# Kernel tuning notes

Hardware: AMD Instinct MI355X
Metric: run time of the kernel (lower is better)

Reference implementation:

```python
import jax, jax.numpy as jnp
import numpy as np


def setup_inputs() -> dict:
    key = jax.random.key(0)
    k1, k2, k3, k4 = jax.random.split(key, 4)
    N, E, F_IN, H, C = 100000, 1600000, 128, 64, 64
    x = jax.random.normal(k1, (N, F_IN), dtype=jnp.float32)
    edge_index = jax.random.randint(k2, (2, E), 0, N, dtype=jnp.int64)
    W1 = jax.random.normal(k3, (F_IN, H), dtype=jnp.float32) / np.sqrt(F_IN)
    b1 = jnp.zeros((H,), dtype=jnp.float32)
    W2 = jax.random.normal(k4, (H, C), dtype=jnp.float32) / np.sqrt(H)
    b2 = jnp.zeros((C,), dtype=jnp.float32)
    return {"x": x, "edge_index": edge_index, "W1": W1, "b1": b1, "W2": W2, "b2": b2}


def reference(x, edge_index, W1, b1, W2, b2):
    N = x.shape[0]
    # add self-loops (PyG GCNConv default)
    loop = jnp.arange(N, dtype=edge_index.dtype)
    src = jnp.concatenate([edge_index[0], loop])
    dst = jnp.concatenate([edge_index[1], loop])
    # symmetric normalization: deg^{-1/2}[src] * deg^{-1/2}[dst], deg over dst
    deg = jax.ops.segment_sum(jnp.ones_like(dst, dtype=x.dtype), dst, num_segments=N)
    dis = jnp.where(deg > 0, jax.lax.rsqrt(deg), 0.0)
    norm = dis[src] * dis[dst]  # [E+N]

    def gcn_conv(h, W, b):
        h = h @ W                                   # [N, out]
        msg = h[src] * norm[:, None]                # [E+N, out] gather
        agg = jax.ops.segment_sum(msg, dst, num_segments=N)  # scatter-add
        return agg + b

    h = jax.nn.relu(gcn_conv(x, W1, b1))
    # dropout inactive in eval mode
    out = gcn_conv(h, W2, b2)
    return jax.nn.log_softmax(out, axis=1)
```

## Files before the change

### kernel.cpp

```cpp
#include <hip/hip_runtime.h>
#include <cstdint>
#include <cstddef>

#define PASSA_EDGES 2048

typedef __attribute__((ext_vector_type(8))) short bf16x8;
typedef __attribute__((ext_vector_type(4))) float f32x4;


__device__ __forceinline__ unsigned short f2bf(float f) {
    unsigned int u = __float_as_uint(f);
    u += 0x7FFFu + ((u >> 16) & 1u);
    return (unsigned short)(u >> 16);
}
__device__ __forceinline__ float bf2f(unsigned short h) {
    return __uint_as_float((unsigned int)h << 16);
}

__device__ __forceinline__ void bf8_fma(uint4 u, float w, float* acc) {
    acc[0] += __uint_as_float(u.x << 16) * w;
    acc[1] += __uint_as_float(u.x & 0xFFFF0000u) * w;
    acc[2] += __uint_as_float(u.y << 16) * w;
    acc[3] += __uint_as_float(u.y & 0xFFFF0000u) * w;
    acc[4] += __uint_as_float(u.z << 16) * w;
    acc[5] += __uint_as_float(u.z & 0xFFFF0000u) * w;
    acc[6] += __uint_as_float(u.w << 16) * w;
    acc[7] += __uint_as_float(u.w & 0xFFFF0000u) * w;
}
__device__ __forceinline__ void bf8_unpack(uint4 u, float* v) {
    v[0] = __uint_as_float(u.x << 16);
    v[1] = __uint_as_float(u.x & 0xFFFF0000u);
    v[2] = __uint_as_float(u.y << 16);
    v[3] = __uint_as_float(u.y & 0xFFFF0000u);
    v[4] = __uint_as_float(u.z << 16);
    v[5] = __uint_as_float(u.z & 0xFFFF0000u);
    v[6] = __uint_as_float(u.w << 16);
    v[7] = __uint_as_float(u.w & 0xFFFF0000u);
}


__global__ void bcur_init(int* __restrict__ bcur, int NBUCK, int CAP) {
    int b = threadIdx.x;
    if (b < NBUCK) bcur[b] = b * CAP;
}


__global__ __launch_bounds__(256) void passA(const int* __restrict__ src,
                                             const int* __restrict__ dst,
                                             int* __restrict__ bcur,
                                             int2* __restrict__ bbuf, int E,
                                             int CAP, int shift) {
    __shared__ int cnt[256], cur[256];
    const int t  = threadIdx.x;
    const int e0 = blockIdx.x * PASSA_EDGES;
    const int n  = min(PASSA_EDGES, E - e0);

    cnt[t] = 0;
    __syncthreads();
    for (int i = t; i < n; i += 256) atomicAdd(&cnt[dst[e0 + i] >> shift], 1);
    __syncthreads();

    const int c = cnt[t];
    cur[t] = (c > 0) ? atomicAdd(&bcur[t], c) : 0;
    __syncthreads();

    for (int i = t; i < n; i += 256) {
        const int d = dst[e0 + i];
        const int s = src[e0 + i];
        const int b = d >> shift;
        const int p = atomicAdd(&cur[b], 1);
        if (p < (b + 1) * CAP) bbuf[p] = make_int2(s, d);
    }
}


__global__ __launch_bounds__(256) void hist_dis(const int2* __restrict__ bbuf,
                                                const int* __restrict__ bcur,
                                                int* __restrict__ hist,
                                                int N, int CAP, int shift) {
    __shared__ int cnt[1024];
    const int b     = blockIdx.x;
    const int node0 = b << shift;
    const int nn    = min(1 << shift, N - node0);
    for (int j = threadIdx.x; j < nn; j += 256) cnt[j] = 0;
    __syncthreads();
    const int start = b * CAP;
    const int end   = min(bcur[b], (b + 1) * CAP);
    for (int e = start + threadIdx.x; e < end; e += 256)
        atomicAdd(&cnt[bbuf[e].y - node0], 1);
    __syncthreads();
    for (int j = threadIdx.x; j < nn; j += 256) hist[node0 + j] = cnt[j];
}


__global__ __launch_bounds__(256) void scan_partial(const int* __restrict__ hist,
                                                    int* __restrict__ partials,
                                                    float* __restrict__ dis, int N) {
    __shared__ int red[256];
    const int t    = threadIdx.x;
    const int base = blockIdx.x * 1024 + t * 4;
    int s = 0;
    if (base + 3 < N) {
        int4 v = *(const int4*)&hist[base];
        s = ((v.x + 7) & ~7) + ((v.y + 7) & ~7) + ((v.z + 7) & ~7) + ((v.w + 7) & ~7);
        dis[base]     = rsqrtf((float)(v.x + 1));
        dis[base + 1] = rsqrtf((float)(v.y + 1));
        dis[base + 2] = rsqrtf((float)(v.z + 1));
        dis[base + 3] = rsqrtf((float)(v.w + 1));
    } else {
        for (int i = 0; i < 4; i++)
            if (base + i < N) {
                int c = hist[base + i];
                s += (c + 7) & ~7;
                dis[base + i] = rsqrtf((float)(c + 1));
            }
    }
    red[t] = s;
    __syncthreads();
    for (int off = 128; off; off >>= 1) {
        if (t < off) red[t] += red[t + off];
        __syncthreads();
    }
    if (t == 0) partials[blockIdx.x] = red[0];
}

__global__ __launch_bounds__(256) void scan_offsets(int* __restrict__ partials, int NB) {
    __shared__ int tmp[256];
    const int t = threadIdx.x;
    int v = (t < NB) ? partials[t] : 0;
    tmp[t] = v;
    __syncthreads();
    for (int off = 1; off < 256; off <<= 1) {
        int u = (t >= off) ? tmp[t - off] : 0;
        __syncthreads();
        tmp[t] += u;
        __syncthreads();
    }
    if (t < NB) partials[t] = tmp[t] - v;
}

__global__ __launch_bounds__(256) void scan_apply(const int* __restrict__ hist,
                                                  const int* __restrict__ partials,
                                                  int* __restrict__ ptr, int N) {
    __shared__ int tsum[256];
    const int t    = threadIdx.x;
    const int base = blockIdx.x * 1024 + t * 4;
    int v[4];
    int s = 0;
    for (int i = 0; i < 4; i++) {
        int c = (base + i < N) ? hist[base + i] : 0;
        v[i]  = (c + 7) & ~7;
        s += v[i];
    }
    tsum[t] = s;
    __syncthreads();
    for (int off = 1; off < 256; off <<= 1) {
        int u = (t >= off) ? tsum[t - off] : 0;
        __syncthreads();
        tsum[t] += u;
        __syncthreads();
    }
    int run = partials[blockIdx.x] + tsum[t] - s;
    for (int i = 0; i < 4; i++) {
        if (base + i < N) {
            ptr[base + i] = run;
            run += v[i];
        }
    }
    if (base <= N - 1 && N - 1 < base + 4) ptr[N] = run;
}


__global__ __launch_bounds__(256) void pad_fill(const int* __restrict__ hist,
                                                const int* __restrict__ ptr,
                                                int2* __restrict__ csrw, int N) {
    const int j = blockIdx.x * 256 + threadIdx.x;
    if (j >= N) return;
    const int t0 = ptr[j] + hist[j];
    const int t1 = ptr[j + 1];
    for (int p = t0; p < t1; ++p) csrw[p] = make_int2(0, 0);
}


__global__ __launch_bounds__(256) void passB(const int2* __restrict__ bbuf,
                                             const int* __restrict__ bcur,
                                             const int* __restrict__ ptr,
                                             int2* __restrict__ csrw,
                                             const float* __restrict__ dis,
                                             int N, int CAP, int shift) {
    __shared__ int lcur[1024];
    const int b     = blockIdx.x;
    const int node0 = b << shift;
    const int nn    = min(1 << shift, N - node0);
    for (int j = threadIdx.x; j < nn; j += 256) lcur[j] = ptr[node0 + j];
    __syncthreads();

    const int start = b * CAP;
    const int end   = min(bcur[b], (b + 1) * CAP);
    for (int e = start + threadIdx.x; e < end; e += 256) {
        const int2 pr = bbuf[e];
        const int  p  = atomicAdd(&lcur[pr.y - node0], 1);
        csrw[p] = make_int2(pr.x, __float_as_int(dis[pr.x]));
    }
}


__global__ __launch_bounds__(256) void prep_wfrag(const float* __restrict__ W1,
                                                  const float* __restrict__ W2,
                                                  unsigned short* __restrict__ whi1,
                                                  unsigned short* __restrict__ wlo1,
                                                  unsigned short* __restrict__ whi2,
                                                  unsigned short* __restrict__ wlo2) {
    for (int e = threadIdx.x; e < 128 * 64; e += 256) {
        const int blk = e >> 9, l = (e >> 3) & 63, j = e & 7;
        const int k = (blk >> 2) * 32 + (l >> 4) * 8 + j;
        const int n = (blk & 3) * 16 + (l & 15);
        const float v = W1[k * 64 + n];
        const unsigned short h = f2bf(v);
        whi1[e] = h;
        wlo1[e] = f2bf(v - bf2f(h));
    }
    for (int e = threadIdx.x; e < 64 * 64; e += 256) {
        const int blk = e >> 9, l = (e >> 3) & 63, j = e & 7;
        const int k = (blk >> 2) * 32 + (l >> 4) * 8 + j;
        const int n = (blk & 3) * 16 + (l & 15);
        const float v = W2[k * 64 + n];
        const unsigned short h = f2bf(v);
        whi2[e] = h;
        wlo2[e] = f2bf(v - bf2f(h));
    }
}


template <int K>
__global__ __launch_bounds__(256) void gemm_mfma(const float* __restrict__ X,
                                                 const unsigned short* __restrict__ whi,
                                                 const unsigned short* __restrict__ wlo,
                                                 unsigned short* __restrict__ Yb, int N) {
    constexpr int LDX = K + 4;
    __shared__ float xs[64 * LDX];
    const int tid  = threadIdx.x;
    const int row0 = blockIdx.x * 64;

#pragma unroll
    for (int i = 0; i < (64 * K) / 1024; ++i) {
        const int fidx = i * 1024 + tid * 4;
        const int r = fidx / K, c = fidx % K;
        const float4 v = *(const float4*)(X + (size_t)min(row0 + r, N - 1) * K + c);
        *(float4*)&xs[r * LDX + c] = v;
    }
    __syncthreads();

    const int w = tid >> 6, l = tid & 63;
    const int m = l & 15, kg = l >> 4;

    f32x4 acc[4] = {};
    const float* xrow = &xs[(w * 16 + m) * LDX];

#pragma unroll
    for (int s = 0; s < K / 32; ++s) {
        const float4 a0 = *(const float4*)(xrow + s * 32 + kg * 8);
        const float4 a1 = *(const float4*)(xrow + s * 32 + kg * 8 + 4);
        const float av[8] = {a0.x, a0.y, a0.z, a0.w, a1.x, a1.y, a1.z, a1.w};
        bf16x8 ahi, alo;
#pragma unroll
        for (int j = 0; j < 8; ++j) {
            const unsigned short h = f2bf(av[j]);
            ahi[j] = (short)h;
            alo[j] = (short)f2bf(av[j] - bf2f(h));
        }
#pragma unroll
        for (int nt = 0; nt < 4; ++nt) {
            const bf16x8 bh = *(const bf16x8*)&whi[(s * 4 + nt) * 512 + l * 8];
            const bf16x8 bl = *(const bf16x8*)&wlo[(s * 4 + nt) * 512 + l * 8];
            acc[nt] = __builtin_amdgcn_mfma_f32_16x16x32_bf16(ahi, bh, acc[nt], 0, 0, 0);
            acc[nt] = __builtin_amdgcn_mfma_f32_16x16x32_bf16(alo, bh, acc[nt], 0, 0, 0);
            acc[nt] = __builtin_amdgcn_mfma_f32_16x16x32_bf16(ahi, bl, acc[nt], 0, 0, 0);
        }
    }

#pragma unroll
    for (int nt = 0; nt < 4; ++nt)
#pragma unroll
        for (int r = 0; r < 4; ++r) {
            const int row = row0 + w * 16 + kg * 4 + r;
            if (row < N) Yb[(size_t)row * 64 + nt * 16 + m] = f2bf(acc[nt][r]);
        }
}


__device__ __forceinline__ void gather8_pad(const unsigned short* __restrict__ B,
                                            const int2* __restrict__ csrw,
                                            int s0, int iters, int co, float* acc) {
    const int4* cs = (const int4*)(csrw + s0);
    int4 c0 = make_int4(0, 0, 0, 0), c1 = c0, c2 = c0, c3 = c0;
    if (iters > 0) { c0 = cs[0]; c1 = cs[1]; c2 = cs[2]; c3 = cs[3]; }
    for (int it = 0; it < iters; ++it) {
        const int nb = min(it + 1, iters - 1) * 4;
        int4 n0 = cs[nb], n1 = cs[nb + 1], n2 = cs[nb + 2], n3 = cs[nb + 3];
        uint4 u0 = *(const uint4*)&B[(size_t)c0.x * 64 + co * 8];
        uint4 u1 = *(const uint4*)&B[(size_t)c0.z * 64 + co * 8];
        uint4 u2 = *(const uint4*)&B[(size_t)c1.x * 64 + co * 8];
        uint4 u3 = *(const uint4*)&B[(size_t)c1.z * 64 + co * 8];
        uint4 u4 = *(const uint4*)&B[(size_t)c2.x * 64 + co * 8];
        uint4 u5 = *(const uint4*)&B[(size_t)c2.z * 64 + co * 8];
        uint4 u6 = *(const uint4*)&B[(size_t)c3.x * 64 + co * 8];
        uint4 u7 = *(const uint4*)&B[(size_t)c3.z * 64 + co * 8];
        bf8_fma(u0, __int_as_float(c0.y), acc);
        bf8_fma(u1, __int_as_float(c0.w), acc);
        bf8_fma(u2, __int_as_float(c1.y), acc);
        bf8_fma(u3, __int_as_float(c1.w), acc);
        bf8_fma(u4, __int_as_float(c2.y), acc);
        bf8_fma(u5, __int_as_float(c2.w), acc);
        bf8_fma(u6, __int_as_float(c3.y), acc);
        bf8_fma(u7, __int_as_float(c3.w), acc);
        c0 = n0; c1 = n1; c2 = n2; c3 = n3;
    }
}


__global__ __launch_bounds__(256) void agg_l1(const unsigned short* __restrict__ B,
                                              const int2* __restrict__ csrw,
                                              const int* __restrict__ ptr,
                                              const float* __restrict__ dis,
                                              const float* __restrict__ b1,
                                              float* __restrict__ hs, int N) {
    const int wid  = threadIdx.x >> 6;
    const int lane = threadIdx.x & 63;
    const int eg   = lane >> 3;
    const int co   = lane & 7;

    const int  row = blockIdx.x * 32 + wid * 8 + eg;
    const bool hr  = (row < N);

    const int   s0 = hr ? ptr[row] : 0;
    const int   s1 = hr ? ptr[row + 1] : 0;
    const float di = hr ? dis[row] : 0.f;
    const int   iters = (s1 - s0) >> 3;

    float acc[8] = {};
    gather8_pad(B, csrw, s0, iters, co, acc);

    if (!hr) return;

    uint4 us = *(const uint4*)&B[(size_t)row * 64 + co * 8];
    float bs[8];
    bf8_unpack(us, bs);
    float bb[8];
    *(float4*)&bb[0] = *(const float4*)&b1[co * 8];
    *(float4*)&bb[4] = *(const float4*)&b1[co * 8 + 4];

    float h[8];
#pragma unroll
    for (int i = 0; i < 8; i++)
        h[i] = fmaxf((acc[i] + bs[i] * di) * di + bb[i], 0.f);

    *(float4*)&hs[(size_t)row * 64 + co * 8]     = make_float4(h[0], h[1], h[2], h[3]);
    *(float4*)&hs[(size_t)row * 64 + co * 8 + 4] = make_float4(h[4], h[5], h[6], h[7]);
}


__global__ __launch_bounds__(256) void agg_l2(const unsigned short* __restrict__ B,
                                              const int2* __restrict__ csrw,
                                              const int* __restrict__ ptr,
                                              const float* __restrict__ dis,
                                              const float* __restrict__ b2,
                                              float* __restrict__ out, int N) {
    const int wid  = threadIdx.x >> 6;
    const int lane = threadIdx.x & 63;
    const int eg   = lane >> 3;
    const int co   = lane & 7;

    const int  row = blockIdx.x * 32 + wid * 8 + eg;
    const bool hr  = (row < N);

    const int   s0 = hr ? ptr[row] : 0;
    const int   s1 = hr ? ptr[row + 1] : 0;
    const float di = hr ? dis[row] : 0.f;
    const int   iters = (s1 - s0) >> 3;

    float acc[8] = {};
    gather8_pad(B, csrw, s0, iters, co, acc);

    if (!hr) return;

    uint4 us = *(const uint4*)&B[(size_t)row * 64 + co * 8];
    float bs[8];
    bf8_unpack(us, bs);
    float bb[8];
    *(float4*)&bb[0] = *(const float4*)&b2[co * 8];
    *(float4*)&bb[4] = *(const float4*)&b2[co * 8 + 4];

    float v[8];
#pragma unroll
    for (int i = 0; i < 8; i++) v[i] = (acc[i] + bs[i] * di) * di + bb[i];

    float m = v[0];
#pragma unroll
    for (int i = 1; i < 8; i++) m = fmaxf(m, v[i]);
#pragma unroll
    for (int off = 1; off <= 4; off <<= 1) m = fmaxf(m, __shfl_xor(m, off));
    float s = 0.f;
#pragma unroll
    for (int i = 0; i < 8; i++) s += __expf(v[i] - m);
#pragma unroll
    for (int off = 1; off <= 4; off <<= 1) s += __shfl_xor(s, off);
    float lse = m + __logf(s);

    float4 oa = make_float4(v[0] - lse, v[1] - lse, v[2] - lse, v[3] - lse);
    float4 ob = make_float4(v[4] - lse, v[5] - lse, v[6] - lse, v[7] - lse);
    *(float4*)&out[(size_t)row * 64 + co * 8]     = oa;
    *(float4*)&out[(size_t)row * 64 + co * 8 + 4] = ob;
}


extern "C" void kernel_launch(void* const* d_in, const int* in_sizes, int n_in,
                              void* d_out, int out_size, void* d_ws, size_t ws_size,
                              hipStream_t stream) {
    const float* x   = (const float*)d_in[0];
    const int*   ei  = (const int*)d_in[1];
    const float* W1  = (const float*)d_in[2];
    const float* b1  = (const float*)d_in[3];
    const float* W2  = (const float*)d_in[4];
    const float* b2  = (const float*)d_in[5];
    float*       out = (float*)d_out;

    const int  N   = in_sizes[0] / 128;
    const int  E   = in_sizes[1] / 2;
    const int* src = ei;
    const int* dst = ei + E;
    const int  NB  = (N + 1023) / 1024;

    int shift = 9;
    while (((N - 1) >> shift) >= 256) shift++;
    const int NBUCK = ((N - 1) >> shift) + 1;
    const int CAP   = ((E / NBUCK) * 3 / 2 + 255) & ~255;

    auto align256 = [](size_t v) { return (v + 255) & ~(size_t)255; };
    char*           p        = (char*)d_ws;
    float*          dis      = (float*)p;          p += align256((size_t)N * 4);
    int*            ptr      = (int*)p;            p += align256((size_t)(N + 1) * 4);
    int*            hist     = (int*)p;            p += align256((size_t)N * 4);
    int*            partials = (int*)p;            p += align256((size_t)NB * 4);
    int*            bcur     = (int*)p;            p += align256(256 * 4);
    int2*           csrw     = (int2*)p;           p += align256(((size_t)E + 8 * (size_t)N) * 8);
    int2*           bbuf     = (int2*)p;           p += align256((size_t)NBUCK * CAP * 8);
    unsigned short* xwb      = (unsigned short*)p; p += align256((size_t)N * 64 * 2);
    unsigned short* whi1     = (unsigned short*)p; p += align256(128 * 64 * 2);
    unsigned short* wlo1     = (unsigned short*)p; p += align256(128 * 64 * 2);
    unsigned short* whi2     = (unsigned short*)p; p += align256(64 * 64 * 2);
    unsigned short* wlo2     = (unsigned short*)p; p += align256(64 * 64 * 2);

    float* hs = out;

    bcur_init<<<1, 256, 0, stream>>>(bcur, NBUCK, CAP);
    prep_wfrag<<<1, 256, 0, stream>>>(W1, W2, whi1, wlo1, whi2, wlo2);
    passA<<<(E + PASSA_EDGES - 1) / PASSA_EDGES, 256, 0, stream>>>(src, dst, bcur, bbuf, E, CAP, shift);
    hist_dis<<<NBUCK, 256, 0, stream>>>(bbuf, bcur, hist, N, CAP, shift);
    scan_partial<<<NB, 256, 0, stream>>>(hist, partials, dis, N);
    scan_offsets<<<1, 256, 0, stream>>>(partials, NB);
    scan_apply<<<NB, 256, 0, stream>>>(hist, partials, ptr, N);
    pad_fill<<<(N + 255) / 256, 256, 0, stream>>>(hist, ptr, csrw, N);
    passB<<<NBUCK, 256, 0, stream>>>(bbuf, bcur, ptr, csrw, dis, N, CAP, shift);

    gemm_mfma<128><<<(N + 63) / 64, 256, 0, stream>>>(x, whi1, wlo1, xwb, N);
    agg_l1<<<(N + 31) / 32, 256, 0, stream>>>(xwb, csrw, ptr, dis, b1, hs, N);
    gemm_mfma<64><<<(N + 63) / 64, 256, 0, stream>>>(hs, whi2, wlo2, xwb, N);
    agg_l2<<<(N + 31) / 32, 256, 0, stream>>>(xwb, csrw, ptr, dis, b2, out, N);
}
```

Before: 269.0 us.

## Fuse degree histogram into bucketing pass and padding fill into CSR scatter

The per-node degree histogram is now built with global atomics inside the bucketing pass, which removes the separate hist_dis kernel. The zero padding of CSR rows moves into the tail of passB, which removes pad_fill. Bucket cursors become relative offsets cleared by memset, and the bucketing pass uses 1024 edges per block. This saves two launches and a full re-read of the bucket buffer, at the cost of about 1.6M scattered global atomics on the histogram and more passA blocks.

Result: slower. 327.7 us (+21.9%).

```diff
diff --git a/kernel.cpp b/kernel.cpp
--- a/kernel.cpp
+++ b/kernel.cpp
@@ -2,7 +2,7 @@
 #include <cstdint>
 #include <cstddef>
 
-#define PASSA_EDGES 2048
+#define PASSA_EDGES 1024
 
 typedef __attribute__((ext_vector_type(8))) short bf16x8;
 typedef __attribute__((ext_vector_type(4))) float f32x4;
@@ -39,15 +39,10 @@
 }
 
 
-__global__ void bcur_init(int* __restrict__ bcur, int NBUCK, int CAP) {
-    int b = threadIdx.x;
-    if (b < NBUCK) bcur[b] = b * CAP;
-}
-
-
 __global__ __launch_bounds__(256) void passA(const int* __restrict__ src,
                                              const int* __restrict__ dst,
                                              int* __restrict__ bcur,
+                                             int* __restrict__ hist,
                                              int2* __restrict__ bbuf, int E,
                                              int CAP, int shift) {
     __shared__ int cnt[256], cur[256];
@@ -57,11 +52,15 @@
 
     cnt[t] = 0;
     __syncthreads();
-    for (int i = t; i < n; i += 256) atomicAdd(&cnt[dst[e0 + i] >> shift], 1);
+    for (int i = t; i < n; i += 256) {
+        const int d = dst[e0 + i];
+        atomicAdd(&cnt[d >> shift], 1);
+        atomicAdd(&hist[d], 1);
+    }
     __syncthreads();
 
     const int c = cnt[t];
-    cur[t] = (c > 0) ? atomicAdd(&bcur[t], c) : 0;
+    cur[t] = (c > 0) ? t * CAP + atomicAdd(&bcur[t], c) : 0;
     __syncthreads();
 
     for (int i = t; i < n; i += 256) {
@@ -71,25 +70,6 @@
         const int p = atomicAdd(&cur[b], 1);
         if (p < (b + 1) * CAP) bbuf[p] = make_int2(s, d);
     }
-}
-
-
-__global__ __launch_bounds__(256) void hist_dis(const int2* __restrict__ bbuf,
-                                                const int* __restrict__ bcur,
-                                                int* __restrict__ hist,
-                                                int N, int CAP, int shift) {
-    __shared__ int cnt[1024];
-    const int b     = blockIdx.x;
-    const int node0 = b << shift;
-    const int nn    = min(1 << shift, N - node0);
-    for (int j = threadIdx.x; j < nn; j += 256) cnt[j] = 0;
-    __syncthreads();
-    const int start = b * CAP;
-    const int end   = min(bcur[b], (b + 1) * CAP);
-    for (int e = start + threadIdx.x; e < end; e += 256)
-        atomicAdd(&cnt[bbuf[e].y - node0], 1);
-    __syncthreads();
-    for (int j = threadIdx.x; j < nn; j += 256) hist[node0 + j] = cnt[j];
 }
 
 
@@ -171,17 +151,6 @@
 }
 
 
-__global__ __launch_bounds__(256) void pad_fill(const int* __restrict__ hist,
-                                                const int* __restrict__ ptr,
-                                                int2* __restrict__ csrw, int N) {
-    const int j = blockIdx.x * 256 + threadIdx.x;
-    if (j >= N) return;
-    const int t0 = ptr[j] + hist[j];
-    const int t1 = ptr[j + 1];
-    for (int p = t0; p < t1; ++p) csrw[p] = make_int2(0, 0);
-}
-
-
 __global__ __launch_bounds__(256) void passB(const int2* __restrict__ bbuf,
                                              const int* __restrict__ bcur,
                                              const int* __restrict__ ptr,
@@ -196,11 +165,17 @@
     __syncthreads();
 
     const int start = b * CAP;
-    const int end   = min(bcur[b], (b + 1) * CAP);
+    const int end   = min(b * CAP + bcur[b], (b + 1) * CAP);
     for (int e = start + threadIdx.x; e < end; e += 256) {
         const int2 pr = bbuf[e];
         const int  p  = atomicAdd(&lcur[pr.y - node0], 1);
         csrw[p] = make_int2(pr.x, __float_as_int(dis[pr.x]));
+    }
+    __syncthreads();
+
+    for (int j = threadIdx.x; j < nn; j += 256) {
+        const int t1 = ptr[node0 + j + 1];
+        for (int p = lcur[j]; p < t1; ++p) csrw[p] = make_int2(0, 0);
     }
 }
 
@@ -453,14 +428,13 @@
 
     float* hs = out;
 
-    bcur_init<<<1, 256, 0, stream>>>(bcur, NBUCK, CAP);
+    hipMemsetAsync(hist, 0, (size_t)N * 4, stream);
+    hipMemsetAsync(bcur, 0, 256 * 4, stream);
     prep_wfrag<<<1, 256, 0, stream>>>(W1, W2, whi1, wlo1, whi2, wlo2);
-    passA<<<(E + PASSA_EDGES - 1) / PASSA_EDGES, 256, 0, stream>>>(src, dst, bcur, bbuf, E, CAP, shift);
-    hist_dis<<<NBUCK, 256, 0, stream>>>(bbuf, bcur, hist, N, CAP, shift);
+    passA<<<(E + PASSA_EDGES - 1) / PASSA_EDGES, 256, 0, stream>>>(src, dst, bcur, hist, bbuf, E, CAP, shift);
     scan_partial<<<NB, 256, 0, stream>>>(hist, partials, dis, N);
     scan_offsets<<<1, 256, 0, stream>>>(partials, NB);
     scan_apply<<<NB, 256, 0, stream>>>(hist, partials, ptr, N);
-    pad_fill<<<(N + 255) / 256, 256, 0, stream>>>(hist, ptr, csrw, N);
     passB<<<NBUCK, 256, 0, stream>>>(bbuf, bcur, ptr, csrw, dis, N, CAP, shift);
 
     gemm_mfma<128><<<(N + 63) / 64, 256, 0, stream>>>(x, whi1, wlo1, xwb, N);
```
